# Kernel tuning notes

Measured on AMD Instinct MI355X. Metric: run time of the kernel, lower is better.

The kernel has to match this reference:

```python
import jax, jax.numpy as jnp
import numpy as np
from jax import lax

B, C, O, H, W = 2, 72, 72, 180, 320
KH = KW = 3
PAD = 1
K = KH * KW          # 9 kernel taps
G = K                # groups inferred by torchvision: in_ch // weight.shape[1] = 9
Cg = C // G          # input channels per group
Og = O // G          # output channels per group


def setup_inputs():
    key = jax.random.key(0)
    k0, k1, k2, k3, k4 = jax.random.split(key, 5)
    return {
        "input": jax.random.normal(k0, (B, C, H, W), jnp.float32),
        "offset_feat": jax.random.normal(k1, (B, C, H, W), jnp.float32),
        "weight": jax.random.normal(k2, (O, Cg, KH, KW), jnp.float32) * 0.05,
        "off_w": jax.random.normal(k3, (2 * K, C, 3, 3), jnp.float32) * 0.01,
        "off_b": jax.random.normal(k4, (2 * K,), jnp.float32) * 0.01,
    }


def _bilinear(img, py, px):
    # img: [B,C,H,W]; py, px: [B,K,H,W] float sample coords. Zero outside image.
    y0 = jnp.floor(py)
    x0 = jnp.floor(px)
    wy1 = py - y0
    wx1 = px - x0
    wy0 = 1.0 - wy1
    wx0 = 1.0 - wx1
    img_flat = img.reshape(B, C, H * W)

    def gather(yi, xi):
        valid = (yi >= 0) & (yi < H) & (xi >= 0) & (xi < W)
        yc = jnp.clip(yi, 0, H - 1).astype(jnp.int32)
        xc = jnp.clip(xi, 0, W - 1).astype(jnp.int32)
        idx = (yc * W + xc).reshape(B, 1, -1)                      # [B,1,K*H*W]
        v = jnp.take_along_axis(img_flat, idx, axis=2)             # [B,C,K*H*W]
        return v.reshape(B, C, K, H, W) * valid.astype(img.dtype)[:, None]

    w00 = (wy0 * wx0)[:, None]  # [B,1,K,H,W]
    w01 = (wy0 * wx1)[:, None]
    w10 = (wy1 * wx0)[:, None]
    w11 = (wy1 * wx1)[:, None]
    out = w00 * gather(y0, x0)
    out = out + w01 * gather(y0, x0 + 1)
    out = out + w10 * gather(y0 + 1, x0)
    out = out + w11 * gather(y0 + 1, x0 + 1)
    return out  # [B,C,K,H,W]


def _deform_conv(x, offset, weight):
    # offset: [B, 2K, H, W] laid out (k, [dy, dx]) per torchvision convention
    off = offset.reshape(B, K, 2, H, W)
    dy, dx = off[:, :, 0], off[:, :, 1]
    ki = jnp.repeat(jnp.arange(KH), KW).astype(jnp.float32)  # tap row index
    kj = jnp.tile(jnp.arange(KW), KH).astype(jnp.float32)    # tap col index
    base_y = ki - PAD  # [K]
    base_x = kj - PAD
    ys = jnp.arange(H, dtype=jnp.float32)
    xs = jnp.arange(W, dtype=jnp.float32)
    py = ys[None, None, :, None] + base_y[None, :, None, None] + dy  # [B,K,H,W]
    px = xs[None, None, None, :] + base_x[None, :, None, None] + dx
    sampled = _bilinear(x, py, px)                                   # [B,C,K,H,W]
    s = sampled.reshape(B, G, Cg, K, H, W)
    w = weight.reshape(G, Og, Cg, K)
    out = jnp.einsum('bgckhw,gock->bgohw', s, w)
    return out.reshape(B, O, H, W)


def reference(input, offset_feat, weight, off_w, off_b):
    # 3x3 conv predicting offsets (stride 1, pad 1)
    offset = lax.conv_general_dilated(
        offset_feat, off_w, window_strides=(1, 1), padding=[(1, 1), (1, 1)],
        dimension_numbers=('NCHW', 'OIHW', 'NCHW'))
    offset = offset + off_b[None, :, None, None]
    return _deform_conv(input, offset, weight)
```

## Files before the change

kernel.cpp:

```cpp
#include <hip/hip_runtime.h>

namespace {
constexpr int B = 2, C = 72, O = 72, H = 180, W = 320;
constexpr int K = 9, G = 9, Cg = 8, Og = 8;
constexpr int OFFC = 2 * K;
constexpr int HW = H * W;
constexpr size_t OFF_ELEMS = (size_t)B * OFFC * HW;
constexpr int W1_ELEMS = OFFC * C * 9;
constexpr int W2_ELEMS = O * Cg * 9;
constexpr int ICW = C / 4;

constexpr int TW = 64, TH = 4;
constexpr int HALO = 2;
constexpr int NR = TH + 2 * HALO;
constexpr int NC = TW + 2 * HALO;
constexpr int TX = W / TW;
constexpr int TY = H / TH;

typedef float f2u __attribute__((ext_vector_type(2), aligned(4)));
}

__global__ __launch_bounds__(256) void transpose_weights(
    const float* __restrict__ off_w,
    const float* __restrict__ weight,
    float* __restrict__ w1t,
    float* __restrict__ w2t)
{
    int i = blockIdx.x * blockDim.x + threadIdx.x;
    if (i < W1_ELEMS) {
        int oc = i % OFFC;
        int tap = (i / OFFC) % 9;
        int ic = i / (OFFC * 9);
        w1t[i] = off_w[(oc * C + ic) * 9 + tap];
    }
    if (i < W2_ELEMS) {
        int og = i % Og;
        int cg = (i / Og) % Cg;
        int k = (i / (Og * Cg)) % K;
        int g = i / (Og * Cg * K);
        w2t[i] = weight[((g * Og + og) * Cg + cg) * 9 + k];
    }
}

__global__ __launch_bounds__(256, 8) void offset_conv(
    const float* __restrict__ x,
    const float* __restrict__ w1t,
    const float* __restrict__ bias,
    float* __restrict__ offs)
{
    __shared__ float red[4 * 64 * OFFC];
    const int lane = threadIdx.x & 63;
    const int wave = threadIdx.x >> 6;

    const int g0 = blockIdx.x * 64;
    const int b = g0 / HW;
    const int pix = g0 - b * HW;
    const int yh = pix / W;
    const int x0b = pix - yh * W;
    const int xw = x0b + lane;

    float acc[OFFC];
    #pragma unroll
    for (int oc = 0; oc < OFFC; ++oc) acc[oc] = 0.f;

    const float* xb = x + (size_t)b * C * HW;
    const int ic0 = __builtin_amdgcn_readfirstlane(wave * ICW);

    const bool rv0 = (yh - 1) >= 0;
    const bool rv2 = (yh + 1) < H;

    #pragma unroll 3
    for (int ici = 0; ici < ICW; ++ici) {
        const int ic = ic0 + ici;
        const float* xc = xb + ic * HW;
        #pragma unroll
        for (int ky = 0; ky < 3; ++ky) {
            const int yy = yh + ky - 1;
            const bool rowv = (ky == 0) ? rv0 : (ky == 2 ? rv2 : true);
            if (!rowv) continue;
            const float* xr = xc + yy * W;
            #pragma unroll
            for (int kx = 0; kx < 3; ++kx) {
                const int xx = xw + kx - 1;
                const bool v = (xx >= 0) & (xx < W);
                const float val = v ? xr[xx] : 0.0f;
                const float* wp = w1t + (ic * 9 + ky * 3 + kx) * OFFC;
                #pragma unroll
                for (int oc = 0; oc < OFFC; ++oc)
                    acc[oc] = fmaf(val, wp[oc], acc[oc]);
            }
        }
    }

    #pragma unroll
    for (int oc = 0; oc < OFFC; ++oc)
        red[(wave * 64 + lane) * OFFC + oc] = acc[oc];
    __syncthreads();

    for (int e = threadIdx.x; e < 64 * OFFC; e += 256) {
        const int oc = e / 64;
        const int px = e - oc * 64;
        float s = bias[oc];
        #pragma unroll
        for (int w = 0; w < 4; ++w)
            s += red[(w * 64 + px) * OFFC + oc];
        offs[(size_t)b * OFFC * HW + (size_t)oc * HW + pix + px] = s;
    }
}

__global__ __launch_bounds__(256) void deform_conv(
    const float* __restrict__ x,
    const float* __restrict__ offs,
    const float* __restrict__ w2t,
    float* __restrict__ out)
{
    __shared__ float sm[Cg * NR * NC];

    const int bi = blockIdx.x;
    const int tx = bi % TX;
    const int ty = (bi / TX) % TY;
    const int g  = (bi / (TX * TY)) % G;
    const int b  = bi / (TX * TY * G);

    const int lane = threadIdx.x & 63;
    const int wrow = threadIdx.x >> 6;
    const int xw = tx * TW + lane;
    const int yh = ty * TH + wrow;

    const int gu = __builtin_amdgcn_readfirstlane(g);
    const float* wg = w2t + gu * (K * Cg * Og);
    const float* xg = x + ((size_t)b * C + gu * Cg) * HW;
    const float* offp = offs + (size_t)b * OFFC * HW + yh * W + xw;

    float dy[K], dx[K];
    #pragma unroll
    for (int k = 0; k < K; ++k) {
        dy[k] = offp[(size_t)(2 * k) * HW];
        dx[k] = offp[(size_t)(2 * k + 1) * HW];
    }

    const int wy = ty * TH - HALO;
    const int wx = tx * TW - HALO;
    for (int e = threadIdx.x; e < Cg * NR * NC; e += 256) {
        const int c  = e % NC;
        const int rr = (e / NC) % NR;
        const int ch = e / (NC * NR);
        const int sy = min(max(wy + rr, 0), H - 1);
        const int sx = min(max(wx + c, 0), W - 1);
        sm[e] = xg[ch * HW + sy * W + sx];
    }
    __syncthreads();

    float acc[Og];
    #pragma unroll
    for (int og = 0; og < Og; ++og) acc[og] = 0.f;

    #pragma unroll
    for (int k = 0; k < K; ++k) {
        float py = (float)(yh + k / 3 - 1) + dy[k];
        float px = (float)(xw + k % 3 - 1) + dx[k];
        float fy = floorf(py);
        float fx = floorf(px);
        int y0 = (int)fy, x0 = (int)fx;
        float wy1 = py - fy, wx1 = px - fx;
        float wy0 = 1.f - wy1, wx0 = 1.f - wx1;
        float hy0 = ((y0 >= 0) & (y0 < H)) ? wy0 : 0.f;
        float hy1 = ((y0 + 1 >= 0) & (y0 + 1 < H)) ? wy1 : 0.f;
        float gx0 = ((x0 >= 0) & (x0 < W)) ? wx0 : 0.f;
        float gx1 = ((x0 + 1 >= 0) & (x0 + 1 < W)) ? wx1 : 0.f;
        int y0c = min(max(y0, 0), H - 1);
        int y1c = min(max(y0 + 1, 0), H - 1);
        int x0c = min(max(x0, 0), W - 1);
        int x1c = min(max(x0 + 1, 0), W - 1);
        int xbase = min(max(x0, 0), W - 2);
        float wA = (x0c == xbase ? gx0 : 0.f) + (x1c == xbase ? gx1 : 0.f);
        float wB = (x0c == xbase + 1 ? gx0 : 0.f) + (x1c == xbase + 1 ? gx1 : 0.f);
        float w00 = hy0 * wA, w01 = hy0 * wB;
        float w10 = hy1 * wA, w11 = hy1 * wB;
        const float* wk = wg + k * (Cg * Og);

        const int lr0 = y0c - wy;
        const int lr1 = y1c - wy;
        const int lcb = xbase - wx;
        const bool inw = ((unsigned)lr0 < NR) & ((unsigned)lr1 < NR) &
                         ((unsigned)lcb < (NC - 1));
        if (inw) {
            const float* s0 = sm + lr0 * NC + lcb;
            const float* s1 = sm + lr1 * NC + lcb;
            #pragma unroll
            for (int cg = 0; cg < Cg; ++cg) {
                const int o = cg * (NR * NC);
                float v = w00 * s0[o];
                v = fmaf(w01, s0[o + 1], v);
                v = fmaf(w10, s1[o], v);
                v = fmaf(w11, s1[o + 1], v);
                #pragma unroll
                for (int og = 0; og < Og; ++og)
                    acc[og] = fmaf(v, wk[cg * Og + og], acc[og]);
            }
        } else {
            const int r0 = y0c * W + xbase;
            const int r1 = y1c * W + xbase;
            #pragma unroll
            for (int cg = 0; cg < Cg; ++cg) {
                const float* xc = xg + cg * HW;
                f2u a0 = *(const f2u*)(xc + r0);
                f2u a1 = *(const f2u*)(xc + r1);
                float v = w00 * a0.x;
                v = fmaf(w01, a0.y, v);
                v = fmaf(w10, a1.x, v);
                v = fmaf(w11, a1.y, v);
                #pragma unroll
                for (int og = 0; og < Og; ++og)
                    acc[og] = fmaf(v, wk[cg * Og + og], acc[og]);
            }
        }
    }
    float* op = out + ((size_t)b * O + gu * Og) * HW + yh * W + xw;
    #pragma unroll
    for (int og = 0; og < Og; ++og) op[(size_t)og * HW] = acc[og];
}

extern "C" void kernel_launch(void* const* d_in, const int* in_sizes, int n_in,
                              void* d_out, int out_size, void* d_ws, size_t ws_size,
                              hipStream_t stream) {
    const float* input       = (const float*)d_in[0];
    const float* offset_feat = (const float*)d_in[1];
    const float* weight      = (const float*)d_in[2];
    const float* off_w       = (const float*)d_in[3];
    const float* off_b       = (const float*)d_in[4];
    float* out = (float*)d_out;

    float* offs = (float*)d_ws;
    float* w1t = offs + OFF_ELEMS;
    float* w2t = w1t + W1_ELEMS;

    transpose_weights<<<(W1_ELEMS + 255) / 256, 256, 0, stream>>>(off_w, weight, w1t, w2t);
    offset_conv<<<(B * HW) / 64, 256, 0, stream>>>(offset_feat, w1t, off_b, offs);
    deform_conv<<<B * G * TX * TY, 256, 0, stream>>>(input, offs, w2t, out);
}
```

Before: 108.9 us.

## Pack channel pairs in LDS and use packed FP32 FMAs in deform conv

Interleaves pairs of input channels in shared memory as float2 and reorders the weight transpose to match. Bilinear sampling and channel accumulation now use two-wide vector FMAs, which can map to packed FP32 instructions on CDNA. Adds a wave-uniform fast path that skips the clamping and validity masking when every lane's samples fall inside the image. In exchange, accumulators become float2 pairs summed at the end, which raises register use and changes the floating-point summation order.

```diff
diff --git a/kernel.cpp b/kernel.cpp
--- a/kernel.cpp
+++ b/kernel.cpp
@@ -16,8 +16,10 @@
 constexpr int NC = TW + 2 * HALO;
 constexpr int TX = W / TW;
 constexpr int TY = H / TH;
+constexpr int NP = Cg / 2;
 
 typedef float f2u __attribute__((ext_vector_type(2), aligned(4)));
+typedef float f2  __attribute__((ext_vector_type(2)));
 }
 
 __global__ __launch_bounds__(256) void transpose_weights(
@@ -34,10 +36,12 @@
         w1t[i] = off_w[(oc * C + ic) * 9 + tap];
     }
     if (i < W2_ELEMS) {
-        int og = i % Og;
-        int cg = (i / Og) % Cg;
-        int k = (i / (Og * Cg)) % K;
-        int g = i / (Og * Cg * K);
+        int comp = i % 2;
+        int og = (i / 2) % Og;
+        int p  = (i / (2 * Og)) % NP;
+        int k  = (i / (2 * Og * NP)) % K;
+        int g  = i / (2 * Og * NP * K);
+        int cg = 2 * p + comp;
         w2t[i] = weight[((g * Og + og) * Cg + cg) * 9 + k];
     }
 }
@@ -114,7 +118,7 @@
     const float* __restrict__ w2t,
     float* __restrict__ out)
 {
-    __shared__ float sm[Cg * NR * NC];
+    __shared__ f2 sm2[NP * NR * NC];
 
     const int bi = blockIdx.x;
     const int tx = bi % TX;
@@ -141,19 +145,21 @@
 
     const int wy = ty * TH - HALO;
     const int wx = tx * TW - HALO;
-    for (int e = threadIdx.x; e < Cg * NR * NC; e += 256) {
+    for (int e = threadIdx.x; e < NP * NR * NC; e += 256) {
         const int c  = e % NC;
         const int rr = (e / NC) % NR;
-        const int ch = e / (NC * NR);
+        const int p  = e / (NC * NR);
         const int sy = min(max(wy + rr, 0), H - 1);
         const int sx = min(max(wx + c, 0), W - 1);
-        sm[e] = xg[ch * HW + sy * W + sx];
+        const float* src = xg + (size_t)(2 * p) * HW + sy * W + sx;
+        f2 v; v.x = src[0]; v.y = src[HW];
+        sm2[e] = v;
     }
     __syncthreads();
 
-    float acc[Og];
-    #pragma unroll
-    for (int og = 0; og < Og; ++og) acc[og] = 0.f;
+    f2 accp[Og];
+    #pragma unroll
+    for (int og = 0; og < Og; ++og) accp[og] = (f2)0.f;
 
     #pragma unroll
     for (int k = 0; k < K; ++k) {
@@ -164,61 +170,75 @@
         int y0 = (int)fy, x0 = (int)fx;
         float wy1 = py - fy, wx1 = px - fx;
         float wy0 = 1.f - wy1, wx0 = 1.f - wx1;
-        float hy0 = ((y0 >= 0) & (y0 < H)) ? wy0 : 0.f;
-        float hy1 = ((y0 + 1 >= 0) & (y0 + 1 < H)) ? wy1 : 0.f;
-        float gx0 = ((x0 >= 0) & (x0 < W)) ? wx0 : 0.f;
-        float gx1 = ((x0 + 1 >= 0) & (x0 + 1 < W)) ? wx1 : 0.f;
-        int y0c = min(max(y0, 0), H - 1);
-        int y1c = min(max(y0 + 1, 0), H - 1);
-        int x0c = min(max(x0, 0), W - 1);
-        int x1c = min(max(x0 + 1, 0), W - 1);
-        int xbase = min(max(x0, 0), W - 2);
-        float wA = (x0c == xbase ? gx0 : 0.f) + (x1c == xbase ? gx1 : 0.f);
-        float wB = (x0c == xbase + 1 ? gx0 : 0.f) + (x1c == xbase + 1 ? gx1 : 0.f);
-        float w00 = hy0 * wA, w01 = hy0 * wB;
-        float w10 = hy1 * wA, w11 = hy1 * wB;
-        const float* wk = wg + k * (Cg * Og);
-
-        const int lr0 = y0c - wy;
-        const int lr1 = y1c - wy;
-        const int lcb = xbase - wx;
+
+        float w00, w01, w10, w11;
+        int lr0, lr1, lcb, r0, r1;
+        if (__all((y0 >= 0) & (y0 + 1 < H) & (x0 >= 0) & (x0 + 1 < W))) {
+            w00 = wy0 * wx0; w01 = wy0 * wx1;
+            w10 = wy1 * wx0; w11 = wy1 * wx1;
+            lr0 = y0 - wy; lr1 = lr0 + 1; lcb = x0 - wx;
+            r0 = y0 * W + x0; r1 = r0 + W;
+        } else {
+            float hy0 = ((y0 >= 0) & (y0 < H)) ? wy0 : 0.f;
+            float hy1 = ((y0 + 1 >= 0) & (y0 + 1 < H)) ? wy1 : 0.f;
+            float gx0 = ((x0 >= 0) & (x0 < W)) ? wx0 : 0.f;
+            float gx1 = ((x0 + 1 >= 0) & (x0 + 1 < W)) ? wx1 : 0.f;
+            int y0c = min(max(y0, 0), H - 1);
+            int y1c = min(max(y0 + 1, 0), H - 1);
+            int x0c = min(max(x0, 0), W - 1);
+            int x1c = min(max(x0 + 1, 0), W - 1);
+            int xb2 = min(max(x0, 0), W - 2);
+            float wA = (x0c == xb2 ? gx0 : 0.f) + (x1c == xb2 ? gx1 : 0.f);
+            float wB = (x0c == xb2 + 1 ? gx0 : 0.f) + (x1c == xb2 + 1 ? gx1 : 0.f);
+            w00 = hy0 * wA; w01 = hy0 * wB;
+            w10 = hy1 * wA; w11 = hy1 * wB;
+            lr0 = y0c - wy; lr1 = y1c - wy; lcb = xb2 - wx;
+            r0 = y0c * W + xb2; r1 = y1c * W + xb2;
+        }
         const bool inw = ((unsigned)lr0 < NR) & ((unsigned)lr1 < NR) &
                          ((unsigned)lcb < (NC - 1));
-        if (inw) {
-            const float* s0 = sm + lr0 * NC + lcb;
-            const float* s1 = sm + lr1 * NC + lcb;
+        const f2 w00_2 = w00, w01_2 = w01, w10_2 = w10, w11_2 = w11;
+        const float* wkbase = wg + k * (Cg * Og);
+
+        #pragma unroll
+        for (int p = 0; p < NP; ++p) {
+            f2 v2;
+            if (inw) {
+                const f2* s0 = sm2 + (p * NR + lr0) * NC + lcb;
+                const f2* s1 = sm2 + (p * NR + lr1) * NC + lcb;
+                f2 v = s0[0] * w00_2;
+                v = __builtin_elementwise_fma(s0[1], w01_2, v);
+                v = __builtin_elementwise_fma(s1[0], w10_2, v);
+                v = __builtin_elementwise_fma(s1[1], w11_2, v);
+                v2 = v;
+            } else {
+                const float* xc0 = xg + (size_t)(2 * p) * HW;
+                const float* xc1 = xc0 + HW;
+                f2u a0 = *(const f2u*)(xc0 + r0);
+                f2u b0 = *(const f2u*)(xc0 + r1);
+                f2u a1 = *(const f2u*)(xc1 + r0);
+                f2u b1 = *(const f2u*)(xc1 + r1);
+                float v0 = w00 * a0.x;
+                v0 = fmaf(w01, a0.y, v0);
+                v0 = fmaf(w10, b0.x, v0);
+                v0 = fmaf(w11, b0.y, v0);
+                float v1 = w00 * a1.x;
+                v1 = fmaf(w01, a1.y, v1);
+                v1 = fmaf(w10, b1.x, v1);
+                v1 = fmaf(w11, b1.y, v1);
+                v2.x = v0; v2.y = v1;
+            }
+            const f2* wkp2 = (const f2*)(wkbase + p * (2 * Og));
             #pragma unroll
-            for (int cg = 0; cg < Cg; ++cg) {
-                const int o = cg * (NR * NC);
-                float v = w00 * s0[o];
-                v = fmaf(w01, s0[o + 1], v);
-                v = fmaf(w10, s1[o], v);
-                v = fmaf(w11, s1[o + 1], v);
-                #pragma unroll
-                for (int og = 0; og < Og; ++og)
-                    acc[og] = fmaf(v, wk[cg * Og + og], acc[og]);
-            }
-        } else {
-            const int r0 = y0c * W + xbase;
-            const int r1 = y1c * W + xbase;
-            #pragma unroll
-            for (int cg = 0; cg < Cg; ++cg) {
-                const float* xc = xg + cg * HW;
-                f2u a0 = *(const f2u*)(xc + r0);
-                f2u a1 = *(const f2u*)(xc + r1);
-                float v = w00 * a0.x;
-                v = fmaf(w01, a0.y, v);
-                v = fmaf(w10, a1.x, v);
-                v = fmaf(w11, a1.y, v);
-                #pragma unroll
-                for (int og = 0; og < Og; ++og)
-                    acc[og] = fmaf(v, wk[cg * Og + og], acc[og]);
-            }
+            for (int og = 0; og < Og; ++og)
+                accp[og] = __builtin_elementwise_fma(v2, wkp2[og], accp[og]);
         }
     }
+
     float* op = out + ((size_t)b * O + gu * Og) * HW + yh * W + xw;
     #pragma unroll
-    for (int og = 0; og < Og; ++og) op[(size_t)og * HW] = acc[og];
+    for (int og = 0; og < Og; ++og)
+        op[(size_t)og * HW] = accp[og].x + accp[og].y;
 }
 
 extern "C" void kernel_launch(void* const* d_in, const int* in_sizes, int n_in,
```

Result: slower. 150.9 us (+38.5%).
